# Performance work log

Measured on AMD Instinct MI355X. Metric: run time of the kernel, lower is better.

The kernel has to match this reference:

```python
import jax, jax.numpy as jnp
import numpy as np

N = 100000   # nodes
E = 1600000  # edges (avg degree 16)
IN = 128
OUT = 64
NEG_SLOPE = 0.01  # nn.LeakyReLU default


def setup_inputs() -> dict:
    key = jax.random.key(0)
    k1, k2, k3, k4 = jax.random.split(key, 4)
    h = jax.random.normal(k1, (N, IN), dtype=jnp.float32)
    edge_src = jax.random.randint(k2, (E,), 0, N, dtype=jnp.int32)
    edge_dst = jax.random.randint(k3, (E,), 0, N, dtype=jnp.int32)
    W = jax.random.normal(k4, (IN, OUT), dtype=jnp.float32) * (1.0 / np.sqrt(IN))
    b = jnp.zeros((OUT,), dtype=jnp.float32)
    return {"h": h, "W": W, "b": b, "edge_src": edge_src, "edge_dst": edge_dst}


def reference(h, W, b, edge_src, edge_dst):
    # DGL GraphConv, norm='both', allow_zero_in_degree=True (degrees clamped to 1)
    ones = jnp.ones((E,), dtype=h.dtype)
    out_deg = jax.ops.segment_sum(ones, edge_src, num_segments=N)
    in_deg = jax.ops.segment_sum(ones, edge_dst, num_segments=N)
    norm_src = jax.lax.rsqrt(jnp.maximum(out_deg, 1.0))  # [N]
    norm_dst = jax.lax.rsqrt(jnp.maximum(in_deg, 1.0))   # [N]
    # in_dim > out_dim: DGL multiplies by W first to shrink edge traffic
    x = (h * norm_src[:, None]) @ W                       # [N, OUT]
    msgs = x[edge_src]                                    # [E, OUT] gather
    agg = jax.ops.segment_sum(msgs, edge_dst, num_segments=N)  # [N, OUT] scatter-add
    rst = agg * norm_dst[:, None] + b
    # LeakyReLU; dropout is identity in eval mode
    return jnp.where(rst >= 0, rst, NEG_SLOPE * rst)
```

## Files before the change

kernel.cpp:

```cpp
#include <hip/hip_runtime.h>

#define IN_DIM 128
#define OUT_DIM 64
#define NEG_SLOPE 0.01f
#define ECHUNK 4096

typedef __attribute__((ext_vector_type(8))) short short8;
typedef __attribute__((ext_vector_type(4))) float floatx4;

__device__ inline float bf_lo(unsigned u) { union { unsigned i; float f; } c; c.i = u << 16; return c.f; }
__device__ inline float bf_hi(unsigned u) { union { unsigned i; float f; } c; c.i = u & 0xFFFF0000u; return c.f; }
__device__ inline unsigned short f2b(float f) {
    union { float f; unsigned i; } c; c.f = f;
    unsigned u = c.i + 0x7FFFu + ((c.i >> 16) & 1u);
    return (unsigned short)(u >> 16);
}

__global__ __launch_bounds__(256) void hist_kernel(
    const int* __restrict__ es, const int* __restrict__ ed,
    int* __restrict__ cntA_d, int* __restrict__ cntA_s, int E, int nbuck) {
    __shared__ int hd[512];
    __shared__ int hs[512];
    int t = threadIdx.x;
    for (int i = t; i < nbuck; i += 256) { hd[i] = 0; hs[i] = 0; }
    __syncthreads();
    int base = blockIdx.x * ECHUNK;
    for (int i = t * 4; i < ECHUNK; i += 1024) {
        int e = base + i;
        if (e < E) {
            int4 d4 = *(const int4*)(ed + e);
            int4 s4 = *(const int4*)(es + e);
            atomicAdd(&hd[d4.x >> 8], 1); atomicAdd(&hd[d4.y >> 8], 1);
            atomicAdd(&hd[d4.z >> 8], 1); atomicAdd(&hd[d4.w >> 8], 1);
            atomicAdd(&hs[s4.x >> 8], 1); atomicAdd(&hs[s4.y >> 8], 1);
            atomicAdd(&hs[s4.z >> 8], 1); atomicAdd(&hs[s4.w >> 8], 1);
        }
    }
    __syncthreads();
    int row = blockIdx.x * nbuck;
    for (int i = t; i < nbuck; i += 256) {
        cntA_d[row + i] = hd[i];
        cntA_s[row + i] = hs[i];
    }
}

__global__ __launch_bounds__(512) void cntscan_kernel(
    const int* __restrict__ cntA_d, const int* __restrict__ cntA_s,
    int* __restrict__ cntB_d, int* __restrict__ cntB_s,
    int* __restrict__ tot_d, int* __restrict__ tot_s,
    int nchunk, int nbuck) {
    __shared__ int s[512];
    int t = threadIdx.x;
    int bid = blockIdx.x;
    const int* cntA = (bid < nbuck) ? cntA_d : cntA_s;
    int* cntB = (bid < nbuck) ? cntB_d : cntB_s;
    int* tot = (bid < nbuck) ? tot_d : tot_s;
    int b = (bid < nbuck) ? bid : bid - nbuck;
    int v = (t < nchunk) ? cntA[t * nbuck + b] : 0;
    s[t] = v;
    __syncthreads();
    for (int d = 1; d < 512; d <<= 1) {
        int u = (t >= d) ? s[t - d] : 0;
        __syncthreads();
        s[t] += u;
        __syncthreads();
    }
    if (t < nchunk) cntB[b * nchunk + t] = s[t] - v;
    if (t == 511) tot[b] = s[511];
}

__global__ __launch_bounds__(512) void base_kernel(
    const int* __restrict__ tot_d, const int* __restrict__ tot_s,
    int* __restrict__ base_d, int* __restrict__ base_s, int nbuck) {
    __shared__ int s[512];
    int t = threadIdx.x;
    for (int which = 0; which < 2; ++which) {
        const int* tot = which ? tot_s : tot_d;
        int* base = which ? base_s : base_d;
        int v = (t < nbuck) ? tot[t] : 0;
        s[t] = v;
        __syncthreads();
        for (int d = 1; d < 512; d <<= 1) {
            int u = (t >= d) ? s[t - d] : 0;
            __syncthreads();
            s[t] += u;
            __syncthreads();
        }
        if (t < nbuck) base[t] = s[t] - v;
        if (t == nbuck - 1) base[nbuck] = s[t];
        __syncthreads();
    }
}

__global__ __launch_bounds__(256) void binpack_kernel(
    const int* __restrict__ es, const int* __restrict__ ed,
    const int* __restrict__ base_d, const int* __restrict__ base_s,
    const int* __restrict__ cntB_d, const int* __restrict__ cntB_s,
    int* __restrict__ bp_dst, unsigned char* __restrict__ bp_src,
    int E, int nchunk, int nbuck) {
    __shared__ int ld[512];
    __shared__ int ls[512];
    int t = threadIdx.x;
    int c = blockIdx.x;
    for (int i = t; i < nbuck; i += 256) {
        ld[i] = base_d[i] + cntB_d[i * nchunk + c];
        ls[i] = base_s[i] + cntB_s[i * nchunk + c];
    }
    __syncthreads();
    int base = c * ECHUNK;
    for (int i = t * 4; i < ECHUNK; i += 1024) {
        int e = base + i;
        if (e < E) {
            int4 s4 = *(const int4*)(es + e);
            int4 d4 = *(const int4*)(ed + e);
            int pd, ps;
            pd = atomicAdd(&ld[d4.x >> 8], 1); bp_dst[pd] = s4.x | ((d4.x & 255) << 24);
            pd = atomicAdd(&ld[d4.y >> 8], 1); bp_dst[pd] = s4.y | ((d4.y & 255) << 24);
            pd = atomicAdd(&ld[d4.z >> 8], 1); bp_dst[pd] = s4.z | ((d4.z & 255) << 24);
            pd = atomicAdd(&ld[d4.w >> 8], 1); bp_dst[pd] = s4.w | ((d4.w & 255) << 24);
            ps = atomicAdd(&ls[s4.x >> 8], 1); bp_src[ps] = (unsigned char)(s4.x & 255);
            ps = atomicAdd(&ls[s4.y >> 8], 1); bp_src[ps] = (unsigned char)(s4.y & 255);
            ps = atomicAdd(&ls[s4.z >> 8], 1); bp_src[ps] = (unsigned char)(s4.z & 255);
            ps = atomicAdd(&ls[s4.w >> 8], 1); bp_src[ps] = (unsigned char)(s4.w & 255);
        }
    }
}

__global__ __launch_bounds__(256) void srccount_kernel(
    const unsigned char* __restrict__ bp_src, const int* __restrict__ base_s,
    int* __restrict__ ds, int n) {
    __shared__ int cnt[256];
    int t = threadIdx.x;
    int b = blockIdx.x;
    cnt[t] = 0;
    __syncthreads();
    int lo = base_s[b], hi = base_s[b + 1];
    for (int i = lo + t; i < hi; i += 256) atomicAdd(&cnt[bp_src[i]], 1);
    __syncthreads();
    int node = (b << 8) + t;
    if (node < n) ds[node] = cnt[t];
}

__global__ __launch_bounds__(256) void dstfill_kernel(
    const int* __restrict__ bp_dst, const int* __restrict__ base_d,
    int* __restrict__ off, int* __restrict__ csr, int n, int E) {
    __shared__ int cnt[256];
    __shared__ int s[256];
    __shared__ int cur[256];
    int t = threadIdx.x;
    int b = blockIdx.x;
    cnt[t] = 0;
    __syncthreads();
    int lo = base_d[b], hi = base_d[b + 1];
    for (int i = lo + t; i < hi; i += 256)
        atomicAdd(&cnt[(int)((unsigned)bp_dst[i] >> 24)], 1);
    __syncthreads();
    int v = cnt[t];
    s[t] = v;
    __syncthreads();
    for (int d = 1; d < 256; d <<= 1) {
        int u = (t >= d) ? s[t - d] : 0;
        __syncthreads();
        s[t] += u;
        __syncthreads();
    }
    int obase = lo + s[t] - v;
    int node = (b << 8) + t;
    if (node < n) off[node] = obase;
    cur[t] = obase;
    if (b == 0 && t == 0) off[n] = E;
    __syncthreads();
    for (int i = lo + t; i < hi; i += 256) {
        int w = bp_dst[i];
        int src = w & 0xFFFFFF;
        int d = (int)((unsigned)w >> 24);
        int slot = atomicAdd(&cur[d], 1);
        csr[slot] = src;
    }
}

__global__ __launch_bounds__(256) void gemm_kernel(const float* __restrict__ h,
                                                   const float* __restrict__ W,
                                                   const int* __restrict__ ds,
                                                   unsigned short* __restrict__ x, int n) {
    __shared__ unsigned short Wt[OUT_DIM][136];
    int tid = threadIdx.x;

    {
        const float4* W4 = (const float4*)W;
        for (int i = tid; i < IN_DIM * OUT_DIM / 4; i += 256) {
            float4 v = W4[i];
            int k = i >> 4, c = (i & 15) * 4;
            Wt[c + 0][k] = f2b(v.x);
            Wt[c + 1][k] = f2b(v.y);
            Wt[c + 2][k] = f2b(v.z);
            Wt[c + 3][k] = f2b(v.w);
        }
    }
    __syncthreads();

    int wid = tid >> 6, lane = tid & 63;
    int rbase = blockIdx.x * 64 + wid * 16;
    int row = rbase + (lane & 15);
    int kg = lane >> 4;
    int rowc = min(row, n - 1);

    const float* hrow = h + (size_t)rowc * IN_DIM + kg * 8;
    float4 af[8];
#pragma unroll
    for (int ks = 0; ks < 4; ks++) {
        af[2 * ks]     = *(const float4*)(hrow + ks * 32);
        af[2 * ks + 1] = *(const float4*)(hrow + ks * 32 + 4);
    }
    short8 afr[4];
#pragma unroll
    for (int ks = 0; ks < 4; ks++) {
        afr[ks][0] = (short)f2b(af[2 * ks].x);
        afr[ks][1] = (short)f2b(af[2 * ks].y);
        afr[ks][2] = (short)f2b(af[2 * ks].z);
        afr[ks][3] = (short)f2b(af[2 * ks].w);
        afr[ks][4] = (short)f2b(af[2 * ks + 1].x);
        afr[ks][5] = (short)f2b(af[2 * ks + 1].y);
        afr[ks][6] = (short)f2b(af[2 * ks + 1].z);
        afr[ks][7] = (short)f2b(af[2 * ks + 1].w);
    }

    floatx4 acc[4];
#pragma unroll
    for (int gf = 0; gf < 4; gf++) acc[gf] = (floatx4){0.f, 0.f, 0.f, 0.f};

#pragma unroll
    for (int ks = 0; ks < 4; ks++) {
#pragma unroll
        for (int gf = 0; gf < 4; gf++) {
            int col = gf * 16 + (lane & 15);
            short8 bfr = *(const short8*)&Wt[col][ks * 32 + kg * 8];
            acc[gf] = __builtin_amdgcn_mfma_f32_16x16x32_bf16(afr[ks], bfr, acc[gf], 0, 0, 0);
        }
    }

#pragma unroll
    for (int r = 0; r < 4; r++) {
        int orow = rbase + (lane >> 4) * 4 + r;
        if (orow < n) {
            float sc = rsqrtf((float)max(ds[orow], 1));
            unsigned short* xr = x + (size_t)orow * OUT_DIM + (lane & 15);
#pragma unroll
            for (int gf = 0; gf < 4; gf++)
                xr[gf * 16] = f2b(acc[gf][r] * sc);
        }
    }
}

__global__ __launch_bounds__(256) void gather_kernel(const unsigned short* __restrict__ x,
                                                     const int* __restrict__ csr,
                                                     const int* __restrict__ off,
                                                     const float* __restrict__ b,
                                                     float* __restrict__ out, int n) {
    int g = threadIdx.x >> 3;
    int p = threadIdx.x & 7;
    int v = blockIdx.x * 32 + g;
    if (v >= n) return;
    int s0 = off[v], s1 = off[v + 1];
    float a0 = 0.f, a1 = 0.f, a2 = 0.f, a3 = 0.f, a4 = 0.f, a5 = 0.f, a6 = 0.f, a7 = 0.f;
    int j = s0;
    for (; j + 4 <= s1; j += 4) {
        int n0 = csr[j], n1 = csr[j + 1], n2 = csr[j + 2], n3 = csr[j + 3];
        uint4 w0 = ((const uint4*)(x + (size_t)n0 * OUT_DIM))[p];
        uint4 w1 = ((const uint4*)(x + (size_t)n1 * OUT_DIM))[p];
        uint4 w2 = ((const uint4*)(x + (size_t)n2 * OUT_DIM))[p];
        uint4 w3 = ((const uint4*)(x + (size_t)n3 * OUT_DIM))[p];
        a0 += (bf_lo(w0.x) + bf_lo(w1.x)) + (bf_lo(w2.x) + bf_lo(w3.x));
        a1 += (bf_hi(w0.x) + bf_hi(w1.x)) + (bf_hi(w2.x) + bf_hi(w3.x));
        a2 += (bf_lo(w0.y) + bf_lo(w1.y)) + (bf_lo(w2.y) + bf_lo(w3.y));
        a3 += (bf_hi(w0.y) + bf_hi(w1.y)) + (bf_hi(w2.y) + bf_hi(w3.y));
        a4 += (bf_lo(w0.z) + bf_lo(w1.z)) + (bf_lo(w2.z) + bf_lo(w3.z));
        a5 += (bf_hi(w0.z) + bf_hi(w1.z)) + (bf_hi(w2.z) + bf_hi(w3.z));
        a6 += (bf_lo(w0.w) + bf_lo(w1.w)) + (bf_lo(w2.w) + bf_lo(w3.w));
        a7 += (bf_hi(w0.w) + bf_hi(w1.w)) + (bf_hi(w2.w) + bf_hi(w3.w));
    }
    for (; j < s1; j++) {
        uint4 w0 = ((const uint4*)(x + (size_t)csr[j] * OUT_DIM))[p];
        a0 += bf_lo(w0.x); a1 += bf_hi(w0.x);
        a2 += bf_lo(w0.y); a3 += bf_hi(w0.y);
        a4 += bf_lo(w0.z); a5 += bf_hi(w0.z);
        a6 += bf_lo(w0.w); a7 += bf_hi(w0.w);
    }
    float nd = rsqrtf((float)max(s1 - s0, 1));
    float4 b0 = ((const float4*)b)[p * 2];
    float4 b1 = ((const float4*)b)[p * 2 + 1];
    float4 r0, r1;
    r0.x = a0 * nd + b0.x; r0.y = a1 * nd + b0.y;
    r0.z = a2 * nd + b0.z; r0.w = a3 * nd + b0.w;
    r1.x = a4 * nd + b1.x; r1.y = a5 * nd + b1.y;
    r1.z = a6 * nd + b1.z; r1.w = a7 * nd + b1.w;
    r0.x = (r0.x >= 0.f) ? r0.x : NEG_SLOPE * r0.x;
    r0.y = (r0.y >= 0.f) ? r0.y : NEG_SLOPE * r0.y;
    r0.z = (r0.z >= 0.f) ? r0.z : NEG_SLOPE * r0.z;
    r0.w = (r0.w >= 0.f) ? r0.w : NEG_SLOPE * r0.w;
    r1.x = (r1.x >= 0.f) ? r1.x : NEG_SLOPE * r1.x;
    r1.y = (r1.y >= 0.f) ? r1.y : NEG_SLOPE * r1.y;
    r1.z = (r1.z >= 0.f) ? r1.z : NEG_SLOPE * r1.z;
    r1.w = (r1.w >= 0.f) ? r1.w : NEG_SLOPE * r1.w;
    float* orow = out + (size_t)v * OUT_DIM + p * 8;
    *(float4*)orow = r0;
    *(float4*)(orow + 4) = r1;
}

extern "C" void kernel_launch(void* const* d_in, const int* in_sizes, int n_in,
                              void* d_out, int out_size, void* d_ws, size_t ws_size,
                              hipStream_t stream) {
    const float* h = (const float*)d_in[0];
    const float* W = (const float*)d_in[1];
    const float* b = (const float*)d_in[2];
    const int* esrc = (const int*)d_in[3];
    const int* edst = (const int*)d_in[4];
    int n = in_sizes[0] / IN_DIM;
    int E = in_sizes[3];
    float* out = (float*)d_out;

    char* ws = (char*)d_ws;
    int* ds  = (int*)ws;
    int* off = (int*)(ws + (size_t)n * 4);
    int* csr = (int*)(ws + (size_t)n * 8 + 16);
    unsigned short* x = (unsigned short*)(ws + (size_t)n * 8 + 16 + (size_t)E * 4);

    int nchunk = (E + ECHUNK - 1) / ECHUNK;
    int nbuck  = (n + 255) >> 8;

    char* xb = (char*)x;
    int* bp_dst = (int*)xb;
    unsigned char* bp_src = (unsigned char*)(xb + 6600000);
    int* cntA_d = (int*)(xb + 8400000);
    int* cntA_s = (int*)(xb + 9100000);
    int* cntB_d = (int*)(xb + 9800000);
    int* cntB_s = (int*)(xb + 10500000);
    int* tot_d  = (int*)(xb + 11200000);
    int* tot_s  = (int*)(xb + 11210000);
    int* base_d = (int*)(xb + 11220000);
    int* base_s = (int*)(xb + 11230000);

    hist_kernel<<<nchunk, 256, 0, stream>>>(esrc, edst, cntA_d, cntA_s, E, nbuck);
    cntscan_kernel<<<2 * nbuck, 512, 0, stream>>>(cntA_d, cntA_s, cntB_d, cntB_s,
                                                  tot_d, tot_s, nchunk, nbuck);
    base_kernel<<<1, 512, 0, stream>>>(tot_d, tot_s, base_d, base_s, nbuck);
    binpack_kernel<<<nchunk, 256, 0, stream>>>(esrc, edst, base_d, base_s,
                                               cntB_d, cntB_s, bp_dst, bp_src,
                                               E, nchunk, nbuck);
    srccount_kernel<<<nbuck, 256, 0, stream>>>(bp_src, base_s, ds, n);
    dstfill_kernel<<<nbuck, 256, 0, stream>>>(bp_dst, base_d, off, csr, n, E);
    gemm_kernel<<<(n + 63) / 64, 256, 0, stream>>>(h, W, ds, x, n);
    gather_kernel<<<(n + 31) / 32, 256, 0, stream>>>(x, csr, off, b, out, n);
}
```

Baseline: 134.1 us.

## Split projected features into column halves and gather each half separately; merge fill kernels

The bf16 projected features are now stored as two separate 32-column arrays, and the gather runs twice, once per half. Each half is 6.4 MB, so the random-access working set per gather pass is smaller and more likely to stay in cache. The price is reading the CSR indices and offsets twice and paying for an extra launch. Separately, the source-degree count and the destination CSR fill are merged into one kernel to save a launch.

```diff
diff --git a/kernel.cpp b/kernel.cpp
--- a/kernel.cpp
+++ b/kernel.cpp
@@ -126,32 +126,29 @@
     }
 }
 
-__global__ __launch_bounds__(256) void srccount_kernel(
-    const unsigned char* __restrict__ bp_src, const int* __restrict__ base_s,
-    int* __restrict__ ds, int n) {
-    __shared__ int cnt[256];
-    int t = threadIdx.x;
-    int b = blockIdx.x;
-    cnt[t] = 0;
-    __syncthreads();
-    int lo = base_s[b], hi = base_s[b + 1];
-    for (int i = lo + t; i < hi; i += 256) atomicAdd(&cnt[bp_src[i]], 1);
-    __syncthreads();
-    int node = (b << 8) + t;
-    if (node < n) ds[node] = cnt[t];
-}
-
-__global__ __launch_bounds__(256) void dstfill_kernel(
-    const int* __restrict__ bp_dst, const int* __restrict__ base_d,
-    int* __restrict__ off, int* __restrict__ csr, int n, int E) {
+__global__ __launch_bounds__(256) void fill_kernel(
+    const int* __restrict__ bp_dst, const unsigned char* __restrict__ bp_src,
+    const int* __restrict__ base_d, const int* __restrict__ base_s,
+    int* __restrict__ ds, int* __restrict__ off, int* __restrict__ csr,
+    int n, int E) {
     __shared__ int cnt[256];
     __shared__ int s[256];
     __shared__ int cur[256];
     int t = threadIdx.x;
-    int b = blockIdx.x;
+    int bkt = blockIdx.x;
+    int node = (bkt << 8) + t;
+
     cnt[t] = 0;
     __syncthreads();
-    int lo = base_d[b], hi = base_d[b + 1];
+    int lo = base_s[bkt], hi = base_s[bkt + 1];
+    for (int i = lo + t; i < hi; i += 256) atomicAdd(&cnt[bp_src[i]], 1);
+    __syncthreads();
+    if (node < n) ds[node] = cnt[t];
+    __syncthreads();
+
+    cnt[t] = 0;
+    __syncthreads();
+    lo = base_d[bkt]; hi = base_d[bkt + 1];
     for (int i = lo + t; i < hi; i += 256)
         atomicAdd(&cnt[(int)((unsigned)bp_dst[i] >> 24)], 1);
     __syncthreads();
@@ -165,10 +162,9 @@
         __syncthreads();
     }
     int obase = lo + s[t] - v;
-    int node = (b << 8) + t;
     if (node < n) off[node] = obase;
     cur[t] = obase;
-    if (b == 0 && t == 0) off[n] = E;
+    if (bkt == 0 && t == 0) off[n] = E;
     __syncthreads();
     for (int i = lo + t; i < hi; i += 256) {
         int w = bp_dst[i];
@@ -182,7 +178,8 @@
 __global__ __launch_bounds__(256) void gemm_kernel(const float* __restrict__ h,
                                                    const float* __restrict__ W,
                                                    const int* __restrict__ ds,
-                                                   unsigned short* __restrict__ x, int n) {
+                                                   unsigned short* __restrict__ xlo,
+                                                   unsigned short* __restrict__ xhi, int n) {
     __shared__ unsigned short Wt[OUT_DIM][136];
     int tid = threadIdx.x;
 
@@ -244,67 +241,57 @@
         int orow = rbase + (lane >> 4) * 4 + r;
         if (orow < n) {
             float sc = rsqrtf((float)max(ds[orow], 1));
-            unsigned short* xr = x + (size_t)orow * OUT_DIM + (lane & 15);
-#pragma unroll
-            for (int gf = 0; gf < 4; gf++)
-                xr[gf * 16] = f2b(acc[gf][r] * sc);
-        }
-    }
-}
-
-__global__ __launch_bounds__(256) void gather_kernel(const unsigned short* __restrict__ x,
+            int c = lane & 15;
+            unsigned short* xl = xlo + (size_t)orow * 32 + c;
+            unsigned short* xh = xhi + (size_t)orow * 32 + c;
+            xl[0]  = f2b(acc[0][r] * sc);
+            xl[16] = f2b(acc[1][r] * sc);
+            xh[0]  = f2b(acc[2][r] * sc);
+            xh[16] = f2b(acc[3][r] * sc);
+        }
+    }
+}
+
+__global__ __launch_bounds__(256) void gather_kernel(const unsigned short* __restrict__ xp,
                                                      const int* __restrict__ csr,
                                                      const int* __restrict__ off,
                                                      const float* __restrict__ b,
-                                                     float* __restrict__ out, int n) {
+                                                     float* __restrict__ out, int n, int cb) {
     int g = threadIdx.x >> 3;
     int p = threadIdx.x & 7;
     int v = blockIdx.x * 32 + g;
     if (v >= n) return;
     int s0 = off[v], s1 = off[v + 1];
-    float a0 = 0.f, a1 = 0.f, a2 = 0.f, a3 = 0.f, a4 = 0.f, a5 = 0.f, a6 = 0.f, a7 = 0.f;
+    float a0 = 0.f, a1 = 0.f, a2 = 0.f, a3 = 0.f;
     int j = s0;
     for (; j + 4 <= s1; j += 4) {
         int n0 = csr[j], n1 = csr[j + 1], n2 = csr[j + 2], n3 = csr[j + 3];
-        uint4 w0 = ((const uint4*)(x + (size_t)n0 * OUT_DIM))[p];
-        uint4 w1 = ((const uint4*)(x + (size_t)n1 * OUT_DIM))[p];
-        uint4 w2 = ((const uint4*)(x + (size_t)n2 * OUT_DIM))[p];
-        uint4 w3 = ((const uint4*)(x + (size_t)n3 * OUT_DIM))[p];
+        uint2 w0 = *(const uint2*)(xp + (size_t)n0 * 32 + p * 4);
+        uint2 w1 = *(const uint2*)(xp + (size_t)n1 * 32 + p * 4);
+        uint2 w2 = *(const uint2*)(xp + (size_t)n2 * 32 + p * 4);
+        uint2 w3 = *(const uint2*)(xp + (size_t)n3 * 32 + p * 4);
         a0 += (bf_lo(w0.x) + bf_lo(w1.x)) + (bf_lo(w2.x) + bf_lo(w3.x));
         a1 += (bf_hi(w0.x) + bf_hi(w1.x)) + (bf_hi(w2.x) + bf_hi(w3.x));
         a2 += (bf_lo(w0.y) + bf_lo(w1.y)) + (bf_lo(w2.y) + bf_lo(w3.y));
         a3 += (bf_hi(w0.y) + bf_hi(w1.y)) + (bf_hi(w2.y) + bf_hi(w3.y));
-        a4 += (bf_lo(w0.z) + bf_lo(w1.z)) + (bf_lo(w2.z) + bf_lo(w3.z));
-        a5 += (bf_hi(w0.z) + bf_hi(w1.z)) + (bf_hi(w2.z) + bf_hi(w3.z));
-        a6 += (bf_lo(w0.w) + bf_lo(w1.w)) + (bf_lo(w2.w) + bf_lo(w3.w));
-        a7 += (bf_hi(w0.w) + bf_hi(w1.w)) + (bf_hi(w2.w) + bf_hi(w3.w));
     }
     for (; j < s1; j++) {
-        uint4 w0 = ((const uint4*)(x + (size_t)csr[j] * OUT_DIM))[p];
+        uint2 w0 = *(const uint2*)(xp + (size_t)csr[j] * 32 + p * 4);
         a0 += bf_lo(w0.x); a1 += bf_hi(w0.x);
         a2 += bf_lo(w0.y); a3 += bf_hi(w0.y);
-        a4 += bf_lo(w0.z); a5 += bf_hi(w0.z);
-        a6 += bf_lo(w0.w); a7 += bf_hi(w0.w);
     }
     float nd = rsqrtf((float)max(s1 - s0, 1));
-    float4 b0 = ((const float4*)b)[p * 2];
-    float4 b1 = ((const float4*)b)[p * 2 + 1];
-    float4 r0, r1;
-    r0.x = a0 * nd + b0.x; r0.y = a1 * nd + b0.y;
-    r0.z = a2 * nd + b0.z; r0.w = a3 * nd + b0.w;
-    r1.x = a4 * nd + b1.x; r1.y = a5 * nd + b1.y;
-    r1.z = a6 * nd + b1.z; r1.w = a7 * nd + b1.w;
-    r0.x = (r0.x >= 0.f) ? r0.x : NEG_SLOPE * r0.x;
-    r0.y = (r0.y >= 0.f) ? r0.y : NEG_SLOPE * r0.y;
-    r0.z = (r0.z >= 0.f) ? r0.z : NEG_SLOPE * r0.z;
-    r0.w = (r0.w >= 0.f) ? r0.w : NEG_SLOPE * r0.w;
-    r1.x = (r1.x >= 0.f) ? r1.x : NEG_SLOPE * r1.x;
-    r1.y = (r1.y >= 0.f) ? r1.y : NEG_SLOPE * r1.y;
-    r1.z = (r1.z >= 0.f) ? r1.z : NEG_SLOPE * r1.z;
-    r1.w = (r1.w >= 0.f) ? r1.w : NEG_SLOPE * r1.w;
-    float* orow = out + (size_t)v * OUT_DIM + p * 8;
-    *(float4*)orow = r0;
-    *(float4*)(orow + 4) = r1;
+    float4 bb = ((const float4*)b)[(cb >> 2) + p];
+    float4 r;
+    r.x = a0 * nd + bb.x;
+    r.y = a1 * nd + bb.y;
+    r.z = a2 * nd + bb.z;
+    r.w = a3 * nd + bb.w;
+    r.x = (r.x >= 0.f) ? r.x : NEG_SLOPE * r.x;
+    r.y = (r.y >= 0.f) ? r.y : NEG_SLOPE * r.y;
+    r.z = (r.z >= 0.f) ? r.z : NEG_SLOPE * r.z;
+    r.w = (r.w >= 0.f) ? r.w : NEG_SLOPE * r.w;
+    *(float4*)(out + (size_t)v * OUT_DIM + cb + p * 4) = r;
 }
 
 extern "C" void kernel_launch(void* const* d_in, const int* in_sizes, int n_in,
@@ -323,12 +310,13 @@
     int* ds  = (int*)ws;
     int* off = (int*)(ws + (size_t)n * 4);
     int* csr = (int*)(ws + (size_t)n * 8 + 16);
-    unsigned short* x = (unsigned short*)(ws + (size_t)n * 8 + 16 + (size_t)E * 4);
+    char* xb = ws + (size_t)n * 8 + 16 + (size_t)E * 4;
+    unsigned short* xlo = (unsigned short*)xb;
+    unsigned short* xhi = (unsigned short*)(xb + (size_t)n * 64);
 
     int nchunk = (E + ECHUNK - 1) / ECHUNK;
     int nbuck  = (n + 255) >> 8;
 
-    char* xb = (char*)x;
     int* bp_dst = (int*)xb;
     unsigned char* bp_src = (unsigned char*)(xb + 6600000);
     int* cntA_d = (int*)(xb + 8400000);
@@ -347,8 +335,9 @@
     binpack_kernel<<<nchunk, 256, 0, stream>>>(esrc, edst, base_d, base_s,
                                                cntB_d, cntB_s, bp_dst, bp_src,
                                                E, nchunk, nbuck);
-    srccount_kernel<<<nbuck, 256, 0, stream>>>(bp_src, base_s, ds, n);
-    dstfill_kernel<<<nbuck, 256, 0, stream>>>(bp_dst, base_d, off, csr, n, E);
-    gemm_kernel<<<(n + 63) / 64, 256, 0, stream>>>(h, W, ds, x, n);
-    gather_kernel<<<(n + 31) / 32, 256, 0, stream>>>(x, csr, off, b, out, n);
-}
+    fill_kernel<<<nbuck, 256, 0, stream>>>(bp_dst, bp_src, base_d, base_s,
+                                           ds, off, csr, n, E);
+    gemm_kernel<<<(n + 63) / 64, 256, 0, stream>>>(h, W, ds, xlo, xhi, n);
+    gather_kernel<<<(n + 31) / 32, 256, 0, stream>>>(xlo, csr, off, b, out, n, 0);
+    gather_kernel<<<(n + 31) / 32, 256, 0, stream>>>(xhi, csr, off, b, out, n, 32);
+}
```

Result: slower. 138.9 us (+3.6%).

## Fuse degree count into CSR fill and degree-sort nodes for balanced gather

Applied to the files above, without the earlier changes.

Merges the source-degree counting kernel into the destination CSR fill kernel, removing one launch. Inside each 256-node bucket it also counting-sorts nodes by in-degree into a permutation. The gather kernel then walks nodes in that order, so the 8-lane groups within a wavefront see similar edge counts and diverge less. The gather inner loop is unrolled to 8 outstanding loads, with a 2-wide and a single-edge tail. The cost is an extra perm array, an extra prefix scan per bucket, and scattered output writes.

```diff
diff --git a/kernel.cpp b/kernel.cpp
--- a/kernel.cpp
+++ b/kernel.cpp
@@ -126,37 +126,37 @@
     }
 }
 
-__global__ __launch_bounds__(256) void srccount_kernel(
-    const unsigned char* __restrict__ bp_src, const int* __restrict__ base_s,
-    int* __restrict__ ds, int n) {
-    __shared__ int cnt[256];
-    int t = threadIdx.x;
-    int b = blockIdx.x;
-    cnt[t] = 0;
-    __syncthreads();
-    int lo = base_s[b], hi = base_s[b + 1];
-    for (int i = lo + t; i < hi; i += 256) atomicAdd(&cnt[bp_src[i]], 1);
-    __syncthreads();
-    int node = (b << 8) + t;
-    if (node < n) ds[node] = cnt[t];
-}
-
-__global__ __launch_bounds__(256) void dstfill_kernel(
-    const int* __restrict__ bp_dst, const int* __restrict__ base_d,
-    int* __restrict__ off, int* __restrict__ csr, int n, int E) {
+__global__ __launch_bounds__(256) void fill_kernel(
+    const int* __restrict__ bp_dst, const unsigned char* __restrict__ bp_src,
+    const int* __restrict__ base_d, const int* __restrict__ base_s,
+    int* __restrict__ ds, int* __restrict__ off, int* __restrict__ csr,
+    int* __restrict__ sortperm, int n, int E) {
     __shared__ int cnt[256];
     __shared__ int s[256];
     __shared__ int cur[256];
-    int t = threadIdx.x;
-    int b = blockIdx.x;
+    __shared__ int dh[256];
+    __shared__ int dc[256];
+    int t = threadIdx.x;
+    int bkt = blockIdx.x;
+    int node = (bkt << 8) + t;
+    int bsize = min(n - (bkt << 8), 256);
+
     cnt[t] = 0;
     __syncthreads();
-    int lo = base_d[b], hi = base_d[b + 1];
+    int lo = base_s[bkt], hi = base_s[bkt + 1];
+    for (int i = lo + t; i < hi; i += 256) atomicAdd(&cnt[bp_src[i]], 1);
+    __syncthreads();
+    if (node < n) ds[node] = cnt[t];
+    __syncthreads();
+
+    cnt[t] = 0;
+    __syncthreads();
+    lo = base_d[bkt]; hi = base_d[bkt + 1];
     for (int i = lo + t; i < hi; i += 256)
         atomicAdd(&cnt[(int)((unsigned)bp_dst[i] >> 24)], 1);
     __syncthreads();
-    int v = cnt[t];
-    s[t] = v;
+    int deg = cnt[t];
+    s[t] = deg;
     __syncthreads();
     for (int d = 1; d < 256; d <<= 1) {
         int u = (t >= d) ? s[t - d] : 0;
@@ -164,12 +164,31 @@
         s[t] += u;
         __syncthreads();
     }
-    int obase = lo + s[t] - v;
-    int node = (b << 8) + t;
+    int obase = lo + s[t] - deg;
     if (node < n) off[node] = obase;
     cur[t] = obase;
-    if (b == 0 && t == 0) off[n] = E;
-    __syncthreads();
+    if (bkt == 0 && t == 0) off[n] = E;
+
+    dh[t] = 0; dc[t] = 0;
+    __syncthreads();
+    int dcl = min(deg, 255);
+    if (t < bsize) atomicAdd(&dh[dcl], 1);
+    __syncthreads();
+    int v2 = dh[t];
+    s[t] = v2;
+    __syncthreads();
+    for (int d = 1; d < 256; d <<= 1) {
+        int u = (t >= d) ? s[t - d] : 0;
+        __syncthreads();
+        s[t] += u;
+        __syncthreads();
+    }
+    if (t < bsize) {
+        int rank = (s[dcl] - dh[dcl]) + atomicAdd(&dc[dcl], 1);
+        sortperm[(bkt << 8) + rank] = node;
+    }
+    __syncthreads();
+
     for (int i = lo + t; i < hi; i += 256) {
         int w = bp_dst[i];
         int src = w & 0xFFFFFF;
@@ -255,31 +274,38 @@
 __global__ __launch_bounds__(256) void gather_kernel(const unsigned short* __restrict__ x,
                                                      const int* __restrict__ csr,
                                                      const int* __restrict__ off,
+                                                     const int* __restrict__ sortperm,
                                                      const float* __restrict__ b,
                                                      float* __restrict__ out, int n) {
-    int g = threadIdx.x >> 3;
+    int idx = blockIdx.x * 32 + (threadIdx.x >> 3);
+    if (idx >= n) return;
+    int v = sortperm[idx];
     int p = threadIdx.x & 7;
-    int v = blockIdx.x * 32 + g;
-    if (v >= n) return;
     int s0 = off[v], s1 = off[v + 1];
     float a0 = 0.f, a1 = 0.f, a2 = 0.f, a3 = 0.f, a4 = 0.f, a5 = 0.f, a6 = 0.f, a7 = 0.f;
     int j = s0;
-    for (; j + 4 <= s1; j += 4) {
-        int n0 = csr[j], n1 = csr[j + 1], n2 = csr[j + 2], n3 = csr[j + 3];
-        uint4 w0 = ((const uint4*)(x + (size_t)n0 * OUT_DIM))[p];
-        uint4 w1 = ((const uint4*)(x + (size_t)n1 * OUT_DIM))[p];
-        uint4 w2 = ((const uint4*)(x + (size_t)n2 * OUT_DIM))[p];
-        uint4 w3 = ((const uint4*)(x + (size_t)n3 * OUT_DIM))[p];
-        a0 += (bf_lo(w0.x) + bf_lo(w1.x)) + (bf_lo(w2.x) + bf_lo(w3.x));
-        a1 += (bf_hi(w0.x) + bf_hi(w1.x)) + (bf_hi(w2.x) + bf_hi(w3.x));
-        a2 += (bf_lo(w0.y) + bf_lo(w1.y)) + (bf_lo(w2.y) + bf_lo(w3.y));
-        a3 += (bf_hi(w0.y) + bf_hi(w1.y)) + (bf_hi(w2.y) + bf_hi(w3.y));
-        a4 += (bf_lo(w0.z) + bf_lo(w1.z)) + (bf_lo(w2.z) + bf_lo(w3.z));
-        a5 += (bf_hi(w0.z) + bf_hi(w1.z)) + (bf_hi(w2.z) + bf_hi(w3.z));
-        a6 += (bf_lo(w0.w) + bf_lo(w1.w)) + (bf_lo(w2.w) + bf_lo(w3.w));
-        a7 += (bf_hi(w0.w) + bf_hi(w1.w)) + (bf_hi(w2.w) + bf_hi(w3.w));
-    }
-    for (; j < s1; j++) {
+    for (; j + 8 <= s1; j += 8) {
+        uint4 w[8];
+#pragma unroll
+        for (int q = 0; q < 8; q++)
+            w[q] = ((const uint4*)(x + (size_t)csr[j + q] * OUT_DIM))[p];
+#pragma unroll
+        for (int q = 0; q < 8; q++) {
+            a0 += bf_lo(w[q].x); a1 += bf_hi(w[q].x);
+            a2 += bf_lo(w[q].y); a3 += bf_hi(w[q].y);
+            a4 += bf_lo(w[q].z); a5 += bf_hi(w[q].z);
+            a6 += bf_lo(w[q].w); a7 += bf_hi(w[q].w);
+        }
+    }
+    for (; j + 2 <= s1; j += 2) {
+        uint4 w0 = ((const uint4*)(x + (size_t)csr[j] * OUT_DIM))[p];
+        uint4 w1 = ((const uint4*)(x + (size_t)csr[j + 1] * OUT_DIM))[p];
+        a0 += bf_lo(w0.x) + bf_lo(w1.x); a1 += bf_hi(w0.x) + bf_hi(w1.x);
+        a2 += bf_lo(w0.y) + bf_lo(w1.y); a3 += bf_hi(w0.y) + bf_hi(w1.y);
+        a4 += bf_lo(w0.z) + bf_lo(w1.z); a5 += bf_hi(w0.z) + bf_hi(w1.z);
+        a6 += bf_lo(w0.w) + bf_lo(w1.w); a7 += bf_hi(w0.w) + bf_hi(w1.w);
+    }
+    if (j < s1) {
         uint4 w0 = ((const uint4*)(x + (size_t)csr[j] * OUT_DIM))[p];
         a0 += bf_lo(w0.x); a1 += bf_hi(w0.x);
         a2 += bf_lo(w0.y); a3 += bf_hi(w0.y);
@@ -320,15 +346,16 @@
     float* out = (float*)d_out;
 
     char* ws = (char*)d_ws;
-    int* ds  = (int*)ws;
-    int* off = (int*)(ws + (size_t)n * 4);
-    int* csr = (int*)(ws + (size_t)n * 8 + 16);
-    unsigned short* x = (unsigned short*)(ws + (size_t)n * 8 + 16 + (size_t)E * 4);
+    int* ds   = (int*)ws;
+    int* off  = (int*)(ws + (size_t)n * 4);
+    int* perm = (int*)(ws + (size_t)n * 8 + 16);
+    int* csr  = (int*)(ws + (size_t)n * 12 + 16);
+    char* xb  = ws + (size_t)n * 12 + 16 + (size_t)E * 4;
+    unsigned short* x = (unsigned short*)xb;
 
     int nchunk = (E + ECHUNK - 1) / ECHUNK;
     int nbuck  = (n + 255) >> 8;
 
-    char* xb = (char*)x;
     int* bp_dst = (int*)xb;
     unsigned char* bp_src = (unsigned char*)(xb + 6600000);
     int* cntA_d = (int*)(xb + 8400000);
@@ -347,8 +374,8 @@
     binpack_kernel<<<nchunk, 256, 0, stream>>>(esrc, edst, base_d, base_s,
                                                cntB_d, cntB_s, bp_dst, bp_src,
                                                E, nchunk, nbuck);
-    srccount_kernel<<<nbuck, 256, 0, stream>>>(bp_src, base_s, ds, n);
-    dstfill_kernel<<<nbuck, 256, 0, stream>>>(bp_dst, base_d, off, csr, n, E);
+    fill_kernel<<<nbuck, 256, 0, stream>>>(bp_dst, bp_src, base_d, base_s,
+                                           ds, off, csr, perm, n, E);
     gemm_kernel<<<(n + 63) / 64, 256, 0, stream>>>(h, W, ds, x, n);
-    gather_kernel<<<(n + 31) / 32, 256, 0, stream>>>(x, csr, off, b, out, n);
-}
+    gather_kernel<<<(n + 31) / 32, 256, 0, stream>>>(x, csr, off, perm, b, out, n);
+}
```

Result: slower. 147.4 us (+9.9%).
